# Performance work log

Measured on AMD Instinct MI355X. Metric: run time of the kernel, lower is better.

Reference implementation:

```python
import jax, jax.numpy as jnp
import numpy as np

K = 20
NEG_SLOPE = 0.2
BN_EPS = 1e-5


def knn_idx(x, k):
    # x: (B, C, N) -> neighbor indices (B, N, k) by largest negative sq-distance
    xt = jnp.swapaxes(x, 1, 2)                      # (B, N, C)
    inner = 2.0 * jnp.einsum('bic,bjc->bij', xt, xt)
    sq = jnp.sum(xt * xt, axis=-1)                  # (B, N)
    dist = inner - sq[:, :, None] - sq[:, None, :]  # -||xi-xj||^2
    _, idx = jax.lax.top_k(dist, k)
    return idx


def edge_feature(x, src, idx):
    # x: (B, C, N) centers; src: (B, C, M) gather source; idx: (B, N, k)
    xt = jnp.swapaxes(x, 1, 2)                      # (B, N, C)
    st = jnp.swapaxes(src, 1, 2)                    # (B, M, C)
    b = jnp.arange(xt.shape[0])[:, None, None]
    neigh = st[b, idx]                              # (B, N, k, C)
    center = xt[:, :, None, :]                      # (B, N, 1, C)
    feat = jnp.concatenate(
        [neigh - center, jnp.broadcast_to(center, neigh.shape)], axis=-1)
    return jnp.transpose(feat, (0, 3, 1, 2))        # (B, 2C, N, k)


def conv_bn_lrelu(x, w, gamma, beta):
    # 1x1 conv (no bias) + training-mode BatchNorm2d + LeakyReLU(0.2)
    y = jnp.einsum('oc,bcnk->bonk', w, x)
    mean = jnp.mean(y, axis=(0, 2, 3), keepdims=True)
    var = jnp.var(y, axis=(0, 2, 3), keepdims=True)
    y = (y - mean) * jax.lax.rsqrt(var + BN_EPS)
    y = y * gamma[None, :, None, None] + beta[None, :, None, None]
    return jnp.where(y >= 0, y, NEG_SLOPE * y)


def knn_ia_idx(x, y, k):
    # cosine-similarity KNN from x (B,Cx,N) into y (B,Cy,M), normalize over channels
    xn = x / jnp.maximum(jnp.linalg.norm(x, axis=1, keepdims=True), 1e-12)
    yn = y / jnp.maximum(jnp.linalg.norm(y, axis=1, keepdims=True), 1e-12)
    simi = jnp.einsum('bci,bcj->bij', xn, yn)       # (B, N, M)
    _, idx = jax.lax.top_k(simi, k)
    return idx


def setup_inputs() -> dict:
    key = jax.random.key(0)
    ks = jax.random.split(key, 8)
    B, N, M, EMB = 8, 1024, 1024, 512
    x = jax.random.normal(ks[0], (B, 3, N), dtype=jnp.float32)
    y = jax.random.normal(ks[1], (B, 128, M), dtype=jnp.float32)
    def w(k_, o, c):
        return jax.random.normal(k_, (o, c), dtype=jnp.float32) * (1.0 / np.sqrt(c))
    inp = {
        'x': x, 'y': y,
        'w1': w(ks[2], 64, 6),
        'w2': w(ks[3], 64, 128),
        'w3': w(ks[4], 128, 128),
        'w4': w(ks[5], 256, 256),
        'w5': w(ks[6], EMB, 512),
        'g1': jnp.ones(64), 'b1': jnp.zeros(64),
        'g2': jnp.ones(64), 'b2': jnp.zeros(64),
        'g3': jnp.ones(128), 'b3': jnp.zeros(128),
        'g4': jnp.ones(256), 'b4': jnp.zeros(256),
        'g5': jnp.ones(EMB), 'b5': jnp.zeros(EMB),
    }
    return inp


def reference(x, y, w1, w2, w3, w4, w5, g1, b1, g2, b2, g3, b3, g4, b4, g5, b5):
    # block 1
    h = conv_bn_lrelu(edge_feature(x, x, knn_idx(x, K)), w1, g1, b1)
    x1 = jnp.max(h, axis=-1)                        # (B, 64, N)
    # block 2
    h = conv_bn_lrelu(edge_feature(x1, x1, knn_idx(x1, K)), w2, g2, b2)
    x2 = jnp.max(h, axis=-1)                        # (B, 64, N)
    # block 3
    h = conv_bn_lrelu(edge_feature(x2, x2, knn_idx(x2, K)), w3, g3, b3)
    x3 = jnp.max(h, axis=-1)                        # (B, 128, N)
    # block 4: cross-attention KNN into y (cosine similarity)
    h = conv_bn_lrelu(edge_feature(x3, y, knn_ia_idx(x3, y, K)), w4, g4, b4)
    x4 = jnp.max(h, axis=-1)                        # (B, 256, N)
    # final 1x1 conv + BN + LeakyReLU on concatenated features (512 ch)
    cat = jnp.concatenate([x1, x2, x3, x4], axis=1)  # (B, 512, N)
    out = conv_bn_lrelu(cat[..., None], w5, g5, b5)[..., 0]
    return out                                       # (B, n_emb_dims, N)
```

## Files before the change

kernel.cpp:

```cpp
#include <hip/hip_runtime.h>
#include <hip/hip_bf16.h>

#define KNN 20
#define NEG_SLOPE 0.2f

constexpr int BB = 8;
constexpr int NN = 1024;
constexpr int MM = 1024;

typedef short bf16x8 __attribute__((ext_vector_type(8)));
typedef float f32x4 __attribute__((ext_vector_type(4)));
typedef double f64x4 __attribute__((ext_vector_type(4)));
typedef unsigned long long u64;

__device__ __forceinline__ u64 pack_key64(double d, int j) {
  u64 u = (u64)__double_as_longlong(d);
  u = (u & 0x8000000000000000ULL) ? ~u : (u | 0x8000000000000000ULL);
  return (u & ~(u64)1023) | (u64)(1023 - j);
}

__device__ __forceinline__ void topk20_u64(u64 (&s)[16], int lane, int* op) {
#pragma unroll
  for (int p = 1; p < 16; p <<= 1) {
#pragma unroll
    for (int k = p; k >= 1; k >>= 1) {
#pragma unroll
      for (int j = k % p; j + k < 16; j += 2 * k) {
#pragma unroll
        for (int i = 0; i < k; ++i) {
          int a = j + i, b = j + i + k;
          if (b < 16 && (a / (2 * p)) == (b / (2 * p))) {
            u64 hi = s[a] > s[b] ? s[a] : s[b];
            u64 lo = s[a] > s[b] ? s[b] : s[a];
            s[a] = hi;
            s[b] = lo;
          }
        }
      }
    }
  }
#pragma unroll
  for (int r = 0; r < KNN; ++r) {
    u64 win = s[0];
#pragma unroll
    for (int off = 32; off > 0; off >>= 1) {
      u64 o = __shfl_xor(win, off, 64);
      win = o > win ? o : win;
    }
    if (lane == 0) op[r] = 1023 - (int)(win & (u64)1023);
    if (s[0] == win) {
#pragma unroll
      for (int i = 0; i < 15; ++i) s[i] = s[i + 1];
      s[15] = 0ULL;
    }
  }
}

__global__ void k_probe_mfma(int* __restrict__ rowt, int* __restrict__ colt,
                             int* __restrict__ flag) {
  __shared__ int cnt[256];
  __shared__ int oksh;
  int tid = threadIdx.x;
  if (tid == 0) oksh = 1;
  for (int e = tid; e < 256; e += 64) cnt[e] = 0;
  __syncthreads();
  int lane = tid & 63;
  f64x4 z = {0.0, 0.0, 0.0, 0.0};
  double ai = (double)(lane & 15);
  double p3 = 1.0, p5 = 1.0;
  int kq = lane >> 4;
  for (int t = 0; t < kq; ++t) { p3 *= 3.0; p5 *= 5.0; }
  f64x4 d1 = __builtin_amdgcn_mfma_f64_16x16x4f64(ai, 1.0, z, 0, 0, 0);
  f64x4 d2 = __builtin_amdgcn_mfma_f64_16x16x4f64(1.0, ai, z, 0, 0, 0);
  f64x4 d3 = __builtin_amdgcn_mfma_f64_16x16x4f64(p3, p5, z, 0, 0, 0);
  bool ok = true;
  int ri[4], ci[4];
#pragma unroll
  for (int r = 0; r < 4; ++r) {
    double va = d1[r], vb = d2[r], vp = d3[r];
    int i = (int)(va * 0.25);
    int j = (int)(vb * 0.25);
    bool e_ok = (i >= 0) && (i < 16) && (j >= 0) && (j < 16) &&
                (va == 4.0 * (double)i) && (vb == 4.0 * (double)j) && (vp == 3616.0);
    if (e_ok) {
      atomicAdd(&cnt[i * 16 + j], 1);
    } else {
      ok = false;
      i = 0;
      j = 0;
    }
    ri[r] = i;
    ci[r] = j;
  }
  if (!ok) atomicExch(&oksh, 0);
  __syncthreads();
  bool bij = true;
  for (int e = tid; e < 256; e += 64)
    if (cnt[e] != 1) bij = false;
  if (!bij) atomicExch(&oksh, 0);
  __syncthreads();
#pragma unroll
  for (int r = 0; r < 4; ++r) {
    rowt[lane * 4 + r] = ri[r];
    colt[lane * 4 + r] = ci[r];
  }
  if (tid == 0) *flag = oksh;
}

__global__ __launch_bounds__(256) void k_transpose_d(
    const float* __restrict__ in, double* __restrict__ out, int C, int Np) {
  int total = BB * C * Np;
  for (int t = blockIdx.x * 256 + threadIdx.x; t < total; t += gridDim.x * 256) {
    int c = t % C;
    int n = (t / C) % Np;
    int b = t / (C * Np);
    out[t] = (double)in[((size_t)b * C + c) * Np + n];
  }
}

__global__ __launch_bounds__(256) void k_cvt_bf16(
    const float* __restrict__ in, __hip_bfloat16* __restrict__ out, int n) {
  int i = blockIdx.x * 256 + threadIdx.x;
  if (i < n) out[i] = __float2bfloat16(in[i]);
}

template <int RECIP>
__global__ __launch_bounds__(256) void k_rowsq(
    const double* __restrict__ A, int ld, int C, double* __restrict__ sq) {
  int p = blockIdx.x * 256 + threadIdx.x;
  if (p >= BB * NN) return;
  const double* row = A + (size_t)p * ld;
  double s = 0.0;
  for (int c = 0; c < C; ++c) { double v = row[c]; s += v * v; }
  if (RECIP) {
    sq[p] = 1.0 / fmax(sqrt(s), 1e-12);
  } else {
    sq[p] = s;
  }
}

__global__ __launch_bounds__(256) void k_knn3(
    const double* __restrict__ xs3, const double* __restrict__ sq, int* __restrict__ idx) {
  __shared__ double P[NN * 3];
  int b = blockIdx.x;
  const double* Xb = xs3 + (size_t)b * NN * 3;
  int tid = threadIdx.x;
  for (int t = tid; t < NN * 3; t += 256) P[t] = Xb[t];
  __syncthreads();
  int wave = tid >> 6, lane = tid & 63;
  int i = blockIdx.y * 4 + wave;
  double xi = P[i * 3], yi = P[i * 3 + 1], zi = P[i * 3 + 2];
  double sqi = sq[b * NN + i];
  u64 s[16];
#pragma unroll
  for (int m = 0; m < 16; ++m) {
    int j = m * 64 + lane;
    double d = fma(xi, P[j * 3], 0.0);
    d = fma(yi, P[j * 3 + 1], d);
    d = fma(zi, P[j * 3 + 2], d);
    s[m] = pack_key64(2.0 * d - sqi - sq[b * NN + j], j);
  }
  int* op = idx + ((size_t)b * NN + i) * KNN;
  topk20_u64(s, lane, op);
}

template <int MODE>
__global__ __launch_bounds__(256) void k_gram_u(
    const double* __restrict__ A, int lda, const double* __restrict__ Bm, int ldb,
    const double* __restrict__ sqA, const double* __restrict__ sqB,
    u64* __restrict__ kk, int C, int b0, const int* __restrict__ rowt,
    const int* __restrict__ colt, const int* __restrict__ flag) {
  __shared__ double As[16][66];
  __shared__ double Bs[16][66];
  int bg = b0 + blockIdx.x;
  int bl = blockIdx.x;
  int j0 = blockIdx.y * 64;
  int i0 = blockIdx.z * 64;
  const double* Ab = A + (size_t)bg * NN * lda;
  const double* Bb = Bm + (size_t)bg * MM * ldb;
  int tid = threadIdx.x;
  if (*flag) {
    int lane = tid & 63, w = tid >> 6;
    int lm = lane & 15, lq = lane >> 4;
    f64x4 acc[4] = {};
    for (int c0 = 0; c0 < C; c0 += 16) {
      if (c0) __syncthreads();
      for (int r = 0; r < 4; ++r) {
        int li = tid + r * 256;
        int row = li >> 4, k = li & 15;
        As[k][row] = Ab[(size_t)(i0 + row) * lda + c0 + k];
        Bs[k][row] = Bb[(size_t)(j0 + row) * ldb + c0 + k];
      }
      __syncthreads();
#pragma unroll
      for (int kc = 0; kc < 4; ++kc) {
        double a = As[kc * 4 + lq][w * 16 + lm];
#pragma unroll
        for (int t = 0; t < 4; ++t) {
          double b = Bs[kc * 4 + lq][t * 16 + lm];
          acc[t] = __builtin_amdgcn_mfma_f64_16x16x4f64(a, b, acc[t], 0, 0, 0);
        }
      }
    }
    int rta[4], cta[4];
#pragma unroll
    for (int r = 0; r < 4; ++r) {
      rta[r] = rowt[lane * 4 + r];
      cta[r] = colt[lane * 4 + r];
    }
#pragma unroll
    for (int t = 0; t < 4; ++t) {
#pragma unroll
      for (int r = 0; r < 4; ++r) {
        int i = i0 + w * 16 + rta[r];
        int j = j0 + t * 16 + cta[r];
        double v = acc[t][r];
        if (MODE == 1) v = 2.0 * v - sqA[(size_t)bg * NN + i] - sqB[(size_t)bg * MM + j];
        if (MODE == 2) v = v * sqA[(size_t)bg * NN + i] * sqB[(size_t)bg * MM + j];
        kk[((size_t)bl * NN + i) * MM + j] = pack_key64(v, j);
      }
    }
  } else {
    int tx = tid & 15, ty = tid >> 4;
    double acc[4][4] = {};
    for (int c0 = 0; c0 < C; c0 += 16) {
      if (c0) __syncthreads();
      for (int r = 0; r < 4; ++r) {
        int li = tid + r * 256;
        int row = li >> 4, k = li & 15;
        As[k][row] = Ab[(size_t)(i0 + row) * lda + c0 + k];
        Bs[k][row] = Bb[(size_t)(j0 + row) * ldb + c0 + k];
      }
      __syncthreads();
#pragma unroll
      for (int k = 0; k < 16; ++k) {
        double a_[4], b_[4];
#pragma unroll
        for (int ii = 0; ii < 4; ++ii) a_[ii] = As[k][ty * 4 + ii];
#pragma unroll
        for (int jj = 0; jj < 4; ++jj) b_[jj] = Bs[k][jj * 16 + tx];
#pragma unroll
        for (int ii = 0; ii < 4; ++ii)
#pragma unroll
          for (int jj = 0; jj < 4; ++jj)
            acc[ii][jj] = fma(a_[ii], b_[jj], acc[ii][jj]);
      }
    }
    for (int ii = 0; ii < 4; ++ii) {
      int i = i0 + ty * 4 + ii;
      double qa = sqA[(size_t)bg * NN + i];
      for (int jj = 0; jj < 4; ++jj) {
        int j = j0 + jj * 16 + tx;
        double v = acc[ii][jj];
        if (MODE == 1) v = 2.0 * v - qa - sqB[(size_t)bg * MM + j];
        if (MODE == 2) v = v * qa * sqB[(size_t)bg * MM + j];
        kk[((size_t)bl * NN + i) * MM + j] = pack_key64(v, j);
      }
    }
  }
}

__global__ __launch_bounds__(256) void k_topk(const u64* __restrict__ kk,
                                              int* __restrict__ idx, int b0) {
  int wave = threadIdx.x >> 6;
  int lane = threadIdx.x & 63;
  int bl = blockIdx.x;
  int row = blockIdx.y * 4 + wave;
  const u64* rp = kk + ((size_t)bl * NN + row) * MM;
  u64 s[16];
#pragma unroll
  for (int m = 0; m < 16; ++m) s[m] = rp[m * 64 + lane];
  int* op = idx + ((size_t)(b0 + bl) * NN + row) * KNN;
  topk20_u64(s, lane, op);
}

__global__ __launch_bounds__(256) void k_featmm2(
    const double* __restrict__ src0, int ld0, int Np0,
    const double* __restrict__ src1, int ld1,
    const float* __restrict__ w, int CW,
    double* __restrict__ out0, double* __restrict__ out1, int C, int O) {
  __shared__ double As[16][68];
  __shared__ double Ws[16][68];
  int nbo = O >> 6;
  int b = blockIdx.x;
  int mode = blockIdx.y >= nbo;
  int o0 = (blockIdx.y - (mode ? nbo : 0)) * 64;
  int j0 = blockIdx.z * 64;
  const double* src = mode ? src1 : src0;
  int lds_ = mode ? ld1 : ld0;
  int Np = mode ? NN : Np0;
  double* out = mode ? out1 : out0;
  int tx = threadIdx.x, ty = threadIdx.y;
  int tid = ty * 16 + tx;
  const double* Sb = src + (size_t)b * Np * lds_;
  double acc[4][4] = {};
  for (int c0 = 0; c0 < C; c0 += 16) {
    for (int r = 0; r < 4; ++r) {
      int li = tid + r * 256;
      int row = li >> 4, k = li & 15;
      int c = c0 + k;
      As[k][row] = (c < C) ? Sb[(size_t)(j0 + row) * lds_ + c] : 0.0;
      double wv = 0.0;
      if (c < C) {
        const float* wr = w + (size_t)(o0 + row) * CW;
        wv = (mode == 0) ? (double)wr[c] : ((double)wr[C + c] - (double)wr[c]);
      }
      Ws[k][row] = wv;
    }
    __syncthreads();
#pragma unroll
    for (int k = 0; k < 16; ++k) {
      double a_[4], b_[4];
#pragma unroll
      for (int ii = 0; ii < 4; ++ii) a_[ii] = As[k][ty * 4 + ii];
#pragma unroll
      for (int jj = 0; jj < 4; ++jj) b_[jj] = Ws[k][tx * 4 + jj];
#pragma unroll
      for (int ii = 0; ii < 4; ++ii)
#pragma unroll
        for (int jj = 0; jj < 4; ++jj)
          acc[ii][jj] = fma(a_[ii], b_[jj], acc[ii][jj]);
    }
    __syncthreads();
  }
  for (int ii = 0; ii < 4; ++ii) {
    int j = j0 + ty * 4 + ii;
    double* op = &out[((size_t)b * Np + j) * O + o0 + tx * 4];
    double2 v0, v1;
    v0.x = acc[ii][0];
    v0.y = acc[ii][1];
    v1.x = acc[ii][2];
    v1.y = acc[ii][3];
    *(double2*)op = v0;
    *(double2*)(op + 2) = v1;
  }
}

__global__ __launch_bounds__(256) void k_gemm5_mfma(
    const __hip_bfloat16* __restrict__ cath, const __hip_bfloat16* __restrict__ w5h,
    float* __restrict__ out) {
  int b = blockIdx.x;
  int j0 = blockIdx.y * 16;
  int o0 = blockIdx.z * 64 + (threadIdx.x >> 6) * 16;
  int lane = threadIdx.x & 63;
  int m = lane & 15;
  int quad = lane >> 4;
  const __hip_bfloat16* arow = cath + ((size_t)b * NN + j0 + m) * 512 + quad * 8;
  const __hip_bfloat16* brow = w5h + (size_t)(o0 + m) * 512 + quad * 8;
  f32x4 acc = {0.f, 0.f, 0.f, 0.f};
#pragma unroll
  for (int c0 = 0; c0 < 512; c0 += 32) {
    bf16x8 a = *(const bf16x8*)(arow + c0);
    bf16x8 bb = *(const bf16x8*)(brow + c0);
    acc = __builtin_amdgcn_mfma_f32_16x16x32_bf16(a, bb, acc, 0, 0, 0);
  }
  float* obase = &out[((size_t)b * NN + j0 + quad * 4) * 512 + o0 + m];
#pragma unroll
  for (int r = 0; r < 4; ++r) obase[(size_t)r * 512] = acc[r];
}

__global__ __launch_bounds__(256) void k_gather(
    const double* __restrict__ u, const double* __restrict__ t, const int* __restrict__ idx,
    double* __restrict__ stats, double* __restrict__ mx, int O, int srcNp) {
  __shared__ int lidx[16 * KNN];
  __shared__ double rs[256];
  __shared__ double rq[256];
  int b = blockIdx.x;
  int n0 = blockIdx.y * 16;
  int o0 = blockIdx.z * 64;
  int tid = threadIdx.x;
  int lane = tid & 63, nsl = tid >> 6;
  for (int w = tid; w < 16 * KNN; w += 256)
    lidx[w] = idx[((size_t)b * NN + n0) * KNN + w];
  __syncthreads();
  int oo = o0 + lane;
  double s1 = 0.0, s2 = 0.0;
  for (int ns = nsl; ns < 16; ns += 4) {
    size_t row = (size_t)b * NN + n0 + ns;
    double tv = t[row * O + oo];
    double mxv = -INFINITY;
    double a1 = 0.0, a2 = 0.0;
#pragma unroll
    for (int k = 0; k < KNN; ++k) {
      int j = lidx[ns * KNN + k];
      double yv = u[((size_t)b * srcNp + j) * O + oo] + tv;
      mxv = fmax(mxv, yv);
      a1 += yv;
      a2 = fma(yv, yv, a2);
    }
    mx[row * O + oo] = mxv;
    s1 += a1;
    s2 += a2;
  }
  rs[tid] = s1;
  rq[tid] = s2;
  __syncthreads();
  if (tid < 64) {
    s1 = rs[tid] + rs[tid + 64] + rs[tid + 128] + rs[tid + 192];
    s2 = rq[tid] + rq[tid + 64] + rq[tid + 128] + rq[tid + 192];
    atomicAdd(&stats[o0 + tid], s1);
    atomicAdd(&stats[O + o0 + tid], s2);
  }
}

__global__ void k_bnfin(const double* __restrict__ stats, const float* __restrict__ gamma,
                        const float* __restrict__ beta, double* __restrict__ sc,
                        int O, double cnt) {
  int o = threadIdx.x;
  if (o >= O) return;
  double mean = stats[o] / cnt;
  double var = stats[O + o] / cnt - mean * mean;
  if (var < 0.0) var = 0.0;
  double rstd = 1.0 / sqrt(var + 1e-5);
  double s = (double)gamma[o] * rstd;
  double c = (double)beta[o] - mean * s;
  sc[o] = s;
  sc[O + o] = c;
}

__global__ __launch_bounds__(256) void k_bnapply(
    const double* __restrict__ mx, const double* __restrict__ u, const double* __restrict__ t,
    const int* __restrict__ idx, const double* __restrict__ sc, double* __restrict__ catd,
    __hip_bfloat16* __restrict__ cath, int coff, int O, int srcNp) {
  int i = blockIdx.x * 256 + threadIdx.x;
  int total = BB * NN * O;
  if (i >= total) return;
  int oo = i % O;
  int n = (i / O) % NN;
  int b = i / (O * NN);
  double s = sc[oo], c = sc[O + oo];
  double v;
  if (s >= 0.0) {
    v = mx[i];
  } else {
    double tv = t[i];
    double mn = INFINITY;
    for (int k = 0; k < KNN; ++k) {
      int j = idx[((size_t)b * NN + n) * KNN + k];
      mn = fmin(mn, u[((size_t)b * srcNp + j) * O + oo] + tv);
    }
    v = mn;
  }
  double a = s * v + c;
  a = (a >= 0.0) ? a : 0.2 * a;
  size_t ci = ((size_t)b * NN + n) * 512 + coff + oo;
  cath[ci] = __float2bfloat16((float)a);
  if (coff < 256) catd[((size_t)b * NN + n) * 256 + coff + oo] = a;
}

__global__ __launch_bounds__(256) void k_stats512(
    const float* __restrict__ y5, double* __restrict__ stats) {
  int b = blockIdx.y;
  int n0 = blockIdx.x * 32;
  int tid = threadIdx.x;
  for (int part = 0; part < 2; ++part) {
    int oo = tid + part * 256;
    float a1 = 0.f, a2 = 0.f;
    for (int ns = 0; ns < 32; ++ns) {
      float v = y5[((size_t)b * NN + n0 + ns) * 512 + oo];
      a1 += v;
      a2 = fmaf(v, v, a2);
    }
    atomicAdd(&stats[oo], (double)a1);
    atomicAdd(&stats[512 + oo], (double)a2);
  }
}

__global__ __launch_bounds__(256) void k_final5b(
    const float* __restrict__ y5, const double* __restrict__ sc, float* __restrict__ out) {
  __shared__ float tile[64][65];
  int b = blockIdx.z;
  int n0 = blockIdx.x * 64;
  int o0 = blockIdx.y * 64;
  int tid = threadIdx.x;
  for (int r = 0; r < 16; ++r) {
    int li = tid + r * 256;
    int nl = li >> 6, ol = li & 63;
    float v = y5[((size_t)b * NN + n0 + nl) * 512 + o0 + ol];
    float a = (float)(sc[o0 + ol] * (double)v + sc[512 + o0 + ol]);
    a = (a >= 0.f) ? a : NEG_SLOPE * a;
    tile[nl][ol] = a;
  }
  __syncthreads();
  for (int r = 0; r < 16; ++r) {
    int li = tid + r * 256;
    int ol = li >> 6, nl = li & 63;
    out[((size_t)b * 512 + o0 + ol) * NN + n0 + nl] = tile[nl][ol];
  }
}

extern "C" void kernel_launch(void* const* d_in, const int* in_sizes, int n_in,
                              void* d_out, int out_size, void* d_ws, size_t ws_size,
                              hipStream_t stream) {
  const float* x = (const float*)d_in[0];
  const float* y = (const float*)d_in[1];
  const float* w1 = (const float*)d_in[2];
  const float* w2 = (const float*)d_in[3];
  const float* w3 = (const float*)d_in[4];
  const float* w4 = (const float*)d_in[5];
  const float* w5 = (const float*)d_in[6];
  const float* g1 = (const float*)d_in[7];
  const float* b1 = (const float*)d_in[8];
  const float* g2 = (const float*)d_in[9];
  const float* b2 = (const float*)d_in[10];
  const float* g3 = (const float*)d_in[11];
  const float* b3 = (const float*)d_in[12];
  const float* g4 = (const float*)d_in[13];
  const float* b4 = (const float*)d_in[14];
  const float* g5 = (const float*)d_in[15];
  const float* b5 = (const float*)d_in[16];

  char* base = (char*)d_ws;
  size_t off = 0;
  auto alloc = [&](size_t bytes) -> char* {
    char* p = base + off;
    off += (bytes + 255) & ~(size_t)255;
    return p;
  };
  double* st = (double*)alloc(1024 * 8);
  double* sc = (double*)alloc(1024 * 8);
  double* sq = (double*)alloc((size_t)BB * NN * 8);
  double* rnx = (double*)alloc((size_t)BB * NN * 8);
  double* rny = (double*)alloc((size_t)BB * MM * 8);
  int* idxb = (int*)alloc((size_t)BB * NN * KNN * 4);
  int* rowt = (int*)alloc(256 * 4);
  int* colt = (int*)alloc(256 * 4);
  int* pflag = (int*)alloc(256);
  double* xs3d = (double*)alloc((size_t)BB * NN * 3 * 8);
  double* ysd = (double*)alloc((size_t)BB * MM * 128 * 8);
  double* catd = (double*)alloc((size_t)BB * NN * 256 * 8);
  __hip_bfloat16* cath = (__hip_bfloat16*)alloc((size_t)BB * NN * 512 * 2);
  __hip_bfloat16* w5h = (__hip_bfloat16*)alloc((size_t)512 * 512 * 2);
  double* uu = (double*)alloc((size_t)BB * MM * 256 * 8);
  double* tt = (double*)alloc((size_t)BB * NN * 256 * 8);
  size_t kkBatchBytes = (size_t)NN * MM * 8;
  size_t avail = (ws_size > off) ? (ws_size - off) : 0;
  int CB = (int)(avail / kkBatchBytes);
  if (CB < 1) CB = 1;
  if (CB > BB) CB = BB;
  u64* KK = (u64*)alloc((size_t)CB * kkBatchBytes);
  float* y5 = (float*)uu;
  double* mx = (double*)d_out;
  float* outp = (float*)d_out;

  const dim3 blk2(16, 16);
  const double cntE = (double)BB * NN * KNN;

  auto knn = [&](const double* A, int lda, const double* Bm, int ldb,
                 const double* sa, const double* sb, int C, int mode) {
    for (int b0 = 0; b0 < BB; b0 += CB) {
      int cb = (BB - b0 < CB) ? (BB - b0) : CB;
      dim3 g(cb, MM / 64, NN / 64);
      if (mode == 1)
        k_gram_u<1><<<g, 256, 0, stream>>>(A, lda, Bm, ldb, sa, sb, KK, C, b0, rowt,
                                           colt, pflag);
      else
        k_gram_u<2><<<g, 256, 0, stream>>>(A, lda, Bm, ldb, sa, sb, KK, C, b0, rowt,
                                           colt, pflag);
      k_topk<<<dim3(cb, 256), 256, 0, stream>>>(KK, idxb, b0);
    }
  };

  auto edge_layer = [&](const double* ctr, int ldc, const double* src, int ldsrc,
                        int srcNp, const float* w, int CW, const float* g,
                        const float* bb, int C, int O, int coff) {
    k_featmm2<<<dim3(8, 2 * (O / 64), 16), blk2, 0, stream>>>(src, ldsrc, srcNp, ctr,
                                                              ldc, w, CW, uu, tt, C, O);
    hipMemsetAsync(st, 0, 1024 * 8, stream);
    k_gather<<<dim3(BB, NN / 16, O / 64), 256, 0, stream>>>(uu, tt, idxb, st, mx, O,
                                                            srcNp);
    k_bnfin<<<1, O, 0, stream>>>(st, g, bb, sc, O, cntE);
    k_bnapply<<<(BB * NN * O + 255) / 256, 256, 0, stream>>>(mx, uu, tt, idxb, sc, catd,
                                                             cath, coff, O, srcNp);
  };

  k_probe_mfma<<<1, 64, 0, stream>>>(rowt, colt, pflag);
  k_transpose_d<<<96, 256, 0, stream>>>(x, xs3d, 3, NN);
  k_transpose_d<<<2048, 256, 0, stream>>>(y, ysd, 128, MM);
  k_cvt_bf16<<<1024, 256, 0, stream>>>(w5, w5h, 512 * 512);

  k_rowsq<0><<<32, 256, 0, stream>>>(xs3d, 3, 3, sq);
  k_knn3<<<dim3(BB, 256), 256, 0, stream>>>(xs3d, sq, idxb);
  edge_layer(xs3d, 3, xs3d, 3, NN, w1, 6, g1, b1, 3, 64, 0);

  k_rowsq<0><<<32, 256, 0, stream>>>(catd, 256, 64, sq);
  knn(catd, 256, catd, 256, sq, sq, 64, 1);
  edge_layer(catd, 256, catd, 256, NN, w2, 128, g2, b2, 64, 64, 64);

  k_rowsq<0><<<32, 256, 0, stream>>>(catd + 64, 256, 64, sq);
  knn(catd + 64, 256, catd + 64, 256, sq, sq, 64, 1);
  edge_layer(catd + 64, 256, catd + 64, 256, NN, w3, 128, g3, b3, 64, 128, 128);

  k_rowsq<1><<<32, 256, 0, stream>>>(catd + 128, 256, 128, rnx);
  k_rowsq<1><<<32, 256, 0, stream>>>(ysd, 128, 128, rny);
  knn(catd + 128, 256, ysd, 128, rnx, rny, 128, 2);
  edge_layer(catd + 128, 256, ysd, 128, MM, w4, 256, g4, b4, 128, 256, 256);

  hipMemsetAsync(st, 0, 1024 * 8, stream);
  k_gemm5_mfma<<<dim3(BB, 64, 8), 256, 0, stream>>>(cath, w5h, y5);
  k_stats512<<<dim3(32, 8), 256, 0, stream>>>(y5, st);
  k_bnfin<<<1, 512, 0, stream>>>(st, g5, b5, sc, 512, (double)(BB * NN));
  k_final5b<<<dim3(16, 8, 8), 256, 0, stream>>>(y5, sc, outp);
}
```

Before: 724.1 us.

## Double-buffer gram MFMA tiles, enlarge to 128 rows, add MFMA path to featmm

The gram kernel now computes 128x64 output tiles per block, two accumulator groups per wave reusing each B fragment. Its global loads for the next channel block go through registers into a second shared-memory buffer, overlapping with the current MFMA work. The feature GEMM gains an fp64 MFMA path, gated by the same probe flag, in place of the scalar FMA loop and switches to a 1D 256-thread block. Costs are more registers and shared memory per block and half as many gram blocks.

```diff
diff --git a/kernel.cpp b/kernel.cpp
--- a/kernel.cpp
+++ b/kernel.cpp
@@ -170,84 +170,128 @@
     const double* __restrict__ sqA, const double* __restrict__ sqB,
     u64* __restrict__ kk, int C, int b0, const int* __restrict__ rowt,
     const int* __restrict__ colt, const int* __restrict__ flag) {
-  __shared__ double As[16][66];
-  __shared__ double Bs[16][66];
+  __shared__ double As[2][16][132];
+  __shared__ double Bs[2][16][68];
   int bg = b0 + blockIdx.x;
   int bl = blockIdx.x;
   int j0 = blockIdx.y * 64;
-  int i0 = blockIdx.z * 64;
+  int i0 = blockIdx.z * 128;
   const double* Ab = A + (size_t)bg * NN * lda;
   const double* Bb = Bm + (size_t)bg * MM * ldb;
   int tid = threadIdx.x;
   if (*flag) {
     int lane = tid & 63, w = tid >> 6;
     int lm = lane & 15, lq = lane >> 4;
-    f64x4 acc[4] = {};
+    f64x4 acc[2][4] = {};
+    for (int r = 0; r < 8; ++r) {
+      int li = tid + r * 256;
+      int row = li >> 4, k = li & 15;
+      As[0][k][row] = Ab[(size_t)(i0 + row) * lda + k];
+    }
+    for (int r = 0; r < 4; ++r) {
+      int li = tid + r * 256;
+      int row = li >> 4, k = li & 15;
+      Bs[0][k][row] = Bb[(size_t)(j0 + row) * ldb + k];
+    }
+    __syncthreads();
+    int nblk = C >> 4;
+    for (int cb = 0; cb < nblk; ++cb) {
+      int buf = cb & 1;
+      double ra[8], rb[4];
+      bool pf = (cb + 1 < nblk);
+      if (pf) {
+        int c0 = (cb + 1) << 4;
+        for (int r = 0; r < 8; ++r) {
+          int li = tid + r * 256;
+          int row = li >> 4, k = li & 15;
+          ra[r] = Ab[(size_t)(i0 + row) * lda + c0 + k];
+        }
+        for (int r = 0; r < 4; ++r) {
+          int li = tid + r * 256;
+          int row = li >> 4, k = li & 15;
+          rb[r] = Bb[(size_t)(j0 + row) * ldb + c0 + k];
+        }
+      }
+#pragma unroll
+      for (int kc = 0; kc < 4; ++kc) {
+        double a0 = As[buf][kc * 4 + lq][w * 16 + lm];
+        double a1 = As[buf][kc * 4 + lq][64 + w * 16 + lm];
+#pragma unroll
+        for (int t = 0; t < 4; ++t) {
+          double b = Bs[buf][kc * 4 + lq][t * 16 + lm];
+          acc[0][t] = __builtin_amdgcn_mfma_f64_16x16x4f64(a0, b, acc[0][t], 0, 0, 0);
+          acc[1][t] = __builtin_amdgcn_mfma_f64_16x16x4f64(a1, b, acc[1][t], 0, 0, 0);
+        }
+      }
+      if (pf) {
+        int nb = buf ^ 1;
+        for (int r = 0; r < 8; ++r) {
+          int li = tid + r * 256;
+          int row = li >> 4, k = li & 15;
+          As[nb][k][row] = ra[r];
+        }
+        for (int r = 0; r < 4; ++r) {
+          int li = tid + r * 256;
+          int row = li >> 4, k = li & 15;
+          Bs[nb][k][row] = rb[r];
+        }
+      }
+      __syncthreads();
+    }
+    int rta[4], cta[4];
+#pragma unroll
+    for (int r = 0; r < 4; ++r) {
+      rta[r] = rowt[lane * 4 + r];
+      cta[r] = colt[lane * 4 + r];
+    }
+#pragma unroll
+    for (int g = 0; g < 2; ++g) {
+#pragma unroll
+      for (int t = 0; t < 4; ++t) {
+#pragma unroll
+        for (int r = 0; r < 4; ++r) {
+          int i = i0 + g * 64 + w * 16 + rta[r];
+          int j = j0 + t * 16 + cta[r];
+          double v = acc[g][t][r];
+          if (MODE == 1)
+            v = 2.0 * v - sqA[(size_t)bg * NN + i] - sqB[(size_t)bg * MM + j];
+          if (MODE == 2) v = v * sqA[(size_t)bg * NN + i] * sqB[(size_t)bg * MM + j];
+          kk[((size_t)bl * NN + i) * MM + j] = pack_key64(v, j);
+        }
+      }
+    }
+  } else {
+    int tx = tid & 15, ty = tid >> 4;
+    double acc[8][4] = {};
     for (int c0 = 0; c0 < C; c0 += 16) {
       if (c0) __syncthreads();
+      for (int r = 0; r < 8; ++r) {
+        int li = tid + r * 256;
+        int row = li >> 4, k = li & 15;
+        As[0][k][row] = Ab[(size_t)(i0 + row) * lda + c0 + k];
+      }
       for (int r = 0; r < 4; ++r) {
         int li = tid + r * 256;
         int row = li >> 4, k = li & 15;
-        As[k][row] = Ab[(size_t)(i0 + row) * lda + c0 + k];
-        Bs[k][row] = Bb[(size_t)(j0 + row) * ldb + c0 + k];
+        Bs[0][k][row] = Bb[(size_t)(j0 + row) * ldb + c0 + k];
       }
       __syncthreads();
 #pragma unroll
-      for (int kc = 0; kc < 4; ++kc) {
-        double a = As[kc * 4 + lq][w * 16 + lm];
-#pragma unroll
-        for (int t = 0; t < 4; ++t) {
-          double b = Bs[kc * 4 + lq][t * 16 + lm];
-          acc[t] = __builtin_amdgcn_mfma_f64_16x16x4f64(a, b, acc[t], 0, 0, 0);
-        }
-      }
-    }
-    int rta[4], cta[4];
-#pragma unroll
-    for (int r = 0; r < 4; ++r) {
-      rta[r] = rowt[lane * 4 + r];
-      cta[r] = colt[lane * 4 + r];
-    }
-#pragma unroll
-    for (int t = 0; t < 4; ++t) {
-#pragma unroll
-      for (int r = 0; r < 4; ++r) {
-        int i = i0 + w * 16 + rta[r];
-        int j = j0 + t * 16 + cta[r];
-        double v = acc[t][r];
-        if (MODE == 1) v = 2.0 * v - sqA[(size_t)bg * NN + i] - sqB[(size_t)bg * MM + j];
-        if (MODE == 2) v = v * sqA[(size_t)bg * NN + i] * sqB[(size_t)bg * MM + j];
-        kk[((size_t)bl * NN + i) * MM + j] = pack_key64(v, j);
-      }
-    }
-  } else {
-    int tx = tid & 15, ty = tid >> 4;
-    double acc[4][4] = {};
-    for (int c0 = 0; c0 < C; c0 += 16) {
-      if (c0) __syncthreads();
-      for (int r = 0; r < 4; ++r) {
-        int li = tid + r * 256;
-        int row = li >> 4, k = li & 15;
-        As[k][row] = Ab[(size_t)(i0 + row) * lda + c0 + k];
-        Bs[k][row] = Bb[(size_t)(j0 + row) * ldb + c0 + k];
-      }
-      __syncthreads();
-#pragma unroll
       for (int k = 0; k < 16; ++k) {
-        double a_[4], b_[4];
-#pragma unroll
-        for (int ii = 0; ii < 4; ++ii) a_[ii] = As[k][ty * 4 + ii];
-#pragma unroll
-        for (int jj = 0; jj < 4; ++jj) b_[jj] = Bs[k][jj * 16 + tx];
-#pragma unroll
-        for (int ii = 0; ii < 4; ++ii)
+        double a_[8], b_[4];
+#pragma unroll
+        for (int ii = 0; ii < 8; ++ii) a_[ii] = As[0][k][ty * 8 + ii];
+#pragma unroll
+        for (int jj = 0; jj < 4; ++jj) b_[jj] = Bs[0][k][jj * 16 + tx];
+#pragma unroll
+        for (int ii = 0; ii < 8; ++ii)
 #pragma unroll
           for (int jj = 0; jj < 4; ++jj)
             acc[ii][jj] = fma(a_[ii], b_[jj], acc[ii][jj]);
       }
     }
-    for (int ii = 0; ii < 4; ++ii) {
-      int i = i0 + ty * 4 + ii;
+    for (int ii = 0; ii < 8; ++ii) {
+      int i = i0 + ty * 8 + ii;
       double qa = sqA[(size_t)bg * NN + i];
       for (int jj = 0; jj < 4; ++jj) {
         int j = j0 + jj * 16 + tx;
@@ -278,7 +322,9 @@
     const double* __restrict__ src0, int ld0, int Np0,
     const double* __restrict__ src1, int ld1,
     const float* __restrict__ w, int CW,
-    double* __restrict__ out0, double* __restrict__ out1, int C, int O) {
+    double* __restrict__ out0, double* __restrict__ out1, int C, int O,
+    const int* __restrict__ rowt, const int* __restrict__ colt,
+    const int* __restrict__ flag) {
   __shared__ double As[16][68];
   __shared__ double Ws[16][68];
   int nbo = O >> 6;
@@ -290,49 +336,95 @@
   int lds_ = mode ? ld1 : ld0;
   int Np = mode ? NN : Np0;
   double* out = mode ? out1 : out0;
-  int tx = threadIdx.x, ty = threadIdx.y;
-  int tid = ty * 16 + tx;
+  int tid = threadIdx.x;
   const double* Sb = src + (size_t)b * Np * lds_;
-  double acc[4][4] = {};
-  for (int c0 = 0; c0 < C; c0 += 16) {
+  if (*flag) {
+    int lane = tid & 63, wv = tid >> 6;
+    int lm = lane & 15, lq = lane >> 4;
+    f64x4 acc[4] = {};
+    for (int c0 = 0; c0 < C; c0 += 16) {
+      if (c0) __syncthreads();
+      for (int r = 0; r < 4; ++r) {
+        int li = tid + r * 256;
+        int row = li >> 4, k = li & 15;
+        int c = c0 + k;
+        As[k][row] = (c < C) ? Sb[(size_t)(j0 + row) * lds_ + c] : 0.0;
+        double wvv = 0.0;
+        if (c < C) {
+          const float* wr = w + (size_t)(o0 + row) * CW;
+          wvv = (mode == 0) ? (double)wr[c] : ((double)wr[C + c] - (double)wr[c]);
+        }
+        Ws[k][row] = wvv;
+      }
+      __syncthreads();
+#pragma unroll
+      for (int kc = 0; kc < 4; ++kc) {
+        double a = As[kc * 4 + lq][wv * 16 + lm];
+#pragma unroll
+        for (int t = 0; t < 4; ++t) {
+          double bb = Ws[kc * 4 + lq][t * 16 + lm];
+          acc[t] = __builtin_amdgcn_mfma_f64_16x16x4f64(a, bb, acc[t], 0, 0, 0);
+        }
+      }
+    }
+    int rta[4], cta[4];
+#pragma unroll
     for (int r = 0; r < 4; ++r) {
-      int li = tid + r * 256;
-      int row = li >> 4, k = li & 15;
-      int c = c0 + k;
-      As[k][row] = (c < C) ? Sb[(size_t)(j0 + row) * lds_ + c] : 0.0;
-      double wv = 0.0;
-      if (c < C) {
-        const float* wr = w + (size_t)(o0 + row) * CW;
-        wv = (mode == 0) ? (double)wr[c] : ((double)wr[C + c] - (double)wr[c]);
-      }
-      Ws[k][row] = wv;
-    }
-    __syncthreads();
-#pragma unroll
-    for (int k = 0; k < 16; ++k) {
-      double a_[4], b_[4];
-#pragma unroll
-      for (int ii = 0; ii < 4; ++ii) a_[ii] = As[k][ty * 4 + ii];
-#pragma unroll
-      for (int jj = 0; jj < 4; ++jj) b_[jj] = Ws[k][tx * 4 + jj];
-#pragma unroll
-      for (int ii = 0; ii < 4; ++ii)
-#pragma unroll
-        for (int jj = 0; jj < 4; ++jj)
-          acc[ii][jj] = fma(a_[ii], b_[jj], acc[ii][jj]);
-    }
-    __syncthreads();
-  }
-  for (int ii = 0; ii < 4; ++ii) {
-    int j = j0 + ty * 4 + ii;
-    double* op = &out[((size_t)b * Np + j) * O + o0 + tx * 4];
-    double2 v0, v1;
-    v0.x = acc[ii][0];
-    v0.y = acc[ii][1];
-    v1.x = acc[ii][2];
-    v1.y = acc[ii][3];
-    *(double2*)op = v0;
-    *(double2*)(op + 2) = v1;
+      rta[r] = rowt[lane * 4 + r];
+      cta[r] = colt[lane * 4 + r];
+    }
+#pragma unroll
+    for (int t = 0; t < 4; ++t) {
+#pragma unroll
+      for (int r = 0; r < 4; ++r) {
+        int j = j0 + wv * 16 + rta[r];
+        int o = o0 + t * 16 + cta[r];
+        out[((size_t)b * Np + j) * O + o] = acc[t][r];
+      }
+    }
+  } else {
+    int tx = tid & 15, ty = tid >> 4;
+    double acc[4][4] = {};
+    for (int c0 = 0; c0 < C; c0 += 16) {
+      if (c0) __syncthreads();
+      for (int r = 0; r < 4; ++r) {
+        int li = tid + r * 256;
+        int row = li >> 4, k = li & 15;
+        int c = c0 + k;
+        As[k][row] = (c < C) ? Sb[(size_t)(j0 + row) * lds_ + c] : 0.0;
+        double wvv = 0.0;
+        if (c < C) {
+          const float* wr = w + (size_t)(o0 + row) * CW;
+          wvv = (mode == 0) ? (double)wr[c] : ((double)wr[C + c] - (double)wr[c]);
+        }
+        Ws[k][row] = wvv;
+      }
+      __syncthreads();
+#pragma unroll
+      for (int k = 0; k < 16; ++k) {
+        double a_[4], b_[4];
+#pragma unroll
+        for (int ii = 0; ii < 4; ++ii) a_[ii] = As[k][ty * 4 + ii];
+#pragma unroll
+        for (int jj = 0; jj < 4; ++jj) b_[jj] = Ws[k][tx * 4 + jj];
+#pragma unroll
+        for (int ii = 0; ii < 4; ++ii)
+#pragma unroll
+          for (int jj = 0; jj < 4; ++jj)
+            acc[ii][jj] = fma(a_[ii], b_[jj], acc[ii][jj]);
+      }
+    }
+    for (int ii = 0; ii < 4; ++ii) {
+      int j = j0 + ty * 4 + ii;
+      double* op = &out[((size_t)b * Np + j) * O + o0 + tx * 4];
+      double2 v0, v1;
+      v0.x = acc[ii][0];
+      v0.y = acc[ii][1];
+      v1.x = acc[ii][2];
+      v1.y = acc[ii][3];
+      *(double2*)op = v0;
+      *(double2*)(op + 2) = v1;
+    }
   }
 }
 
@@ -543,14 +635,13 @@
   double* mx = (double*)d_out;
   float* outp = (float*)d_out;
 
-  const dim3 blk2(16, 16);
   const double cntE = (double)BB * NN * KNN;
 
   auto knn = [&](const double* A, int lda, const double* Bm, int ldb,
                  const double* sa, const double* sb, int C, int mode) {
     for (int b0 = 0; b0 < BB; b0 += CB) {
       int cb = (BB - b0 < CB) ? (BB - b0) : CB;
-      dim3 g(cb, MM / 64, NN / 64);
+      dim3 g(cb, MM / 64, NN / 128);
       if (mode == 1)
         k_gram_u<1><<<g, 256, 0, stream>>>(A, lda, Bm, ldb, sa, sb, KK, C, b0, rowt,
                                            colt, pflag);
@@ -564,8 +655,8 @@
   auto edge_layer = [&](const double* ctr, int ldc, const double* src, int ldsrc,
                         int srcNp, const float* w, int CW, const float* g,
                         const float* bb, int C, int O, int coff) {
-    k_featmm2<<<dim3(8, 2 * (O / 64), 16), blk2, 0, stream>>>(src, ldsrc, srcNp, ctr,
-                                                              ldc, w, CW, uu, tt, C, O);
+    k_featmm2<<<dim3(8, 2 * (O / 64), 16), 256, 0, stream>>>(
+        src, ldsrc, srcNp, ctr, ldc, w, CW, uu, tt, C, O, rowt, colt, pflag);
     hipMemsetAsync(st, 0, 1024 * 8, stream);
     k_gather<<<dim3(BB, NN / 16, O / 64), 256, 0, stream>>>(uu, tt, idxb, st, mx, O,
                                                             srcNp);
```

Result: faster. 708.7 us (-2.1%).
